# Kernel tuning notes

Measured on AMD Instinct MI355X. Metric: run time of the kernel, lower is better.

The kernel has to match this reference:

```python
import jax, jax.numpy as jnp
import numpy as np

N, E, G, S = 200000, 800000, 2048, 128
NUM_OPS, NUM_ETYPES, NUMERIC = 64, 4, 12
H, TEXT, VOCAB, OUT = 256, 64, 30000, 512
IN0 = 32 + NUMERIC  # 44


def _ln(h, eps=1e-5):
    # nn.LayerNorm with default (ones/zeros) affine, created fresh each forward
    m = h.mean(-1, keepdims=True)
    v = ((h - m) ** 2).mean(-1, keepdims=True)
    return (h - m) * jax.lax.rsqrt(v + eps)


def _leaky(v):
    return jnp.where(v > 0, v, 0.1 * v)  # LeakyReLU(0.1)


def setup_inputs() -> dict:
    key = jax.random.key(0)
    ks = jax.random.split(key, 40)
    x = jax.random.normal(ks[0], (N, 1 + NUMERIC), jnp.float32)
    x = x.at[:, 0].set(jax.random.randint(ks[1], (N,), 0, NUM_OPS).astype(jnp.float32))
    inp = {
        'x': x,
        'edge_index': jax.random.randint(ks[2], (2, E), 0, N),
        'edge_attr': jax.random.randint(ks[3], (E,), 0, NUM_ETYPES),
        'batch': jnp.sort(jax.random.randint(ks[4], (N,), 0, G)),
        'sql_ids': jax.random.randint(ks[5], (G, S), 0, VOCAB),
        'sql_mask': (jax.random.uniform(ks[6], (G, S)) > 0.3).astype(jnp.float32),
        'op_embed': jax.random.normal(ks[7], (NUM_OPS, 32), jnp.float32),
        'edge_embed': jax.random.normal(ks[8], (NUM_ETYPES, 16), jnp.float32),
        'token_embed': jax.random.normal(ks[9], (VOCAB, TEXT), jnp.float32).at[0].set(0.0),  # padding_idx=0
    }
    dims = [IN0, H, H]
    k = 10
    for i, d in enumerate(dims):
        inp[f'lin_w{i}'] = jax.random.normal(ks[k], (d, 16), jnp.float32) * 0.05; k += 1
        inp[f'lin_b{i}'] = jnp.zeros((d,), jnp.float32)
        inp[f'eps{i}'] = jnp.zeros((), jnp.float32)  # train_eps init 0
        inp[f'W1_{i}'] = jax.random.normal(ks[k], (H, d), jnp.float32) * 0.05; k += 1
        inp[f'b1_{i}'] = jnp.zeros((H,), jnp.float32)
        inp[f'W2_{i}'] = jax.random.normal(ks[k], (H, H), jnp.float32) * 0.05; k += 1
        inp[f'b2_{i}'] = jnp.zeros((H,), jnp.float32)
    inp['mW1'] = jax.random.normal(ks[k], (H, H + 3 + TEXT), jnp.float32) * 0.05; k += 1
    inp['mb1'] = jnp.zeros((H,), jnp.float32)
    inp['mW2'] = jax.random.normal(ks[k], (OUT, H), jnp.float32) * 0.05
    inp['mb2'] = jnp.zeros((OUT,), jnp.float32)
    return inp


def reference(x, edge_index, edge_attr, batch, sql_ids, sql_mask,
              op_embed, edge_embed, token_embed,
              lin_w0, lin_b0, eps0, W1_0, b1_0, W2_0, b2_0,
              lin_w1, lin_b1, eps1, W1_1, b1_1, W2_1, b2_1,
              lin_w2, lin_b2, eps2, W1_2, b1_2, W2_2, b2_2,
              mW1, mb1, mW2, mb2):
    op_ids = jnp.clip(x[:, 0].astype(jnp.int32), 0, NUM_OPS - 1)
    nums = x[:, 1:]
    e_idx = jnp.minimum(edge_attr, NUM_ETYPES - 1)  # clamp_max
    edge_emb = edge_embed[e_idx]                    # [E,16]
    h = jnp.concatenate([op_embed[op_ids], nums], 1)  # [N,44]
    src, dst = edge_index[0], edge_index[1]
    convs = [(lin_w0, lin_b0, eps0, W1_0, b1_0, W2_0, b2_0),
             (lin_w1, lin_b1, eps1, W1_1, b1_1, W2_1, b2_1),
             (lin_w2, lin_b2, eps2, W1_2, b1_2, W2_2, b2_2)]
    for (lw, lb, eps, W1, b1, W2, b2) in convs:
        h_in = h
        # GINEConv: msg = relu(x_j + Lin(edge_attr)); sum-aggregate at dst
        msg = jax.nn.relu(h[src] + edge_emb @ lw.T + lb)        # [E,d]
        aggr = jax.ops.segment_sum(msg, dst, num_segments=h.shape[0])
        z = (1.0 + eps) * h + aggr
        h = jax.nn.relu(z @ W1.T + b1) @ W2.T + b2              # conv MLP -> [N,H]
        h = _ln(h)
        h = _leaky(h + h_in) if h_in.shape[-1] == h.shape[-1] else _leaky(h)
    # graph pooling
    g = jax.ops.segment_sum(h, batch, num_segments=G)            # global_add_pool
    count = jax.ops.segment_sum(jnp.ones((h.shape[0],), h.dtype), batch, num_segments=G)
    denom = jnp.maximum(count, 1.0)                              # scatter_mean semantics
    fanout_mean = jax.ops.segment_sum(x[:, 5], batch, num_segments=G) / denom
    cost_mean = jax.ops.segment_sum(x[:, 4], batch, num_segments=G) / denom
    graph_sum = jnp.stack([count, fanout_mean, cost_mean], 1)    # [G,3]
    # text pooling (masked mean)
    emb = token_embed[sql_ids]                                   # [G,S,TEXT]
    summed = (emb * sql_mask[..., None]).sum(1)
    lengths = jnp.maximum(sql_mask.sum(1, keepdims=True), 1.0)
    text_feat = summed / lengths
    cat = jnp.concatenate([g, graph_sum, text_feat], 1)          # [G, H+3+TEXT]
    hid = _leaky(cat @ mW1.T + mb1)                              # Dropout(0.1) is identity in eval
    return hid @ mW2.T + mb2                                     # [G, OUT]
```

## Files before the change

kernel.cpp:

```cpp
#include <hip/hip_runtime.h>

#define NN 200000
#define EE 800000
#define GG 2048
#define NBLK ((NN + 255) / 256)

typedef __attribute__((ext_vector_type(8))) short short8;
typedef __attribute__((ext_vector_type(4))) float f32x4;

__device__ __forceinline__ float bf2f(ushort u){
  unsigned x = ((unsigned)u) << 16;
  return __uint_as_float(x);
}
__device__ __forceinline__ ushort f2bf(float f){
  unsigned x = __float_as_uint(f);
  x += 0x7fffu + ((x >> 16) & 1u);
  return (ushort)(x >> 16);
}

__device__ __forceinline__ void swz256(const float* __restrict__ W, ushort* __restrict__ o, int idx){
  int ks = idx >> 13, rem = idx & 8191;
  int j16 = rem >> 9, rem2 = rem & 511;
  int ln = rem2 >> 3, t = rem2 & 7;
  int row = j16*16 + (ln & 15);
  int k = ks*32 + (ln >> 4)*8 + t;
  o[idx] = f2bf(W[(size_t)row*256 + k]);
}

__global__ __launch_bounds__(256) void prep_k(
    const float* __restrict__ W10, const float* __restrict__ W20,
    const float* __restrict__ W11, const float* __restrict__ W21,
    const float* __restrict__ W12, const float* __restrict__ W22,
    const float* __restrict__ lw0, const float* __restrict__ lb0,
    const float* __restrict__ lw1, const float* __restrict__ lb1,
    const float* __restrict__ lw2, const float* __restrict__ lb2,
    const float* __restrict__ eE, const float* __restrict__ mW1,
    const float* __restrict__ mW2,
    ushort* __restrict__ wb10, ushort* __restrict__ wb20,
    ushort* __restrict__ wb11, ushort* __restrict__ wb21,
    ushort* __restrict__ wb12, ushort* __restrict__ wb22,
    ushort* __restrict__ mW1b, ushort* __restrict__ mW2b,
    float* __restrict__ eb)
{
  int b = blockIdx.x, tid = threadIdx.x;
  if (b < 64){
    int idx = b*256 + tid;
    int ks = idx >> 13, rem = idx & 8191;
    int j16 = rem >> 9, rem2 = rem & 511;
    int ln = rem2 >> 3, t = rem2 & 7;
    int row = j16*16 + (ln & 15);
    int k = ks*32 + (ln >> 4)*8 + t;
    wb10[idx] = (k < 44) ? f2bf(W10[row*44 + k]) : (ushort)0;
    return;
  }
  b -= 64;
  if (b < 256){ swz256(W20, wb20, b*256+tid); return; } b -= 256;
  if (b < 256){ swz256(W11, wb11, b*256+tid); return; } b -= 256;
  if (b < 256){ swz256(W21, wb21, b*256+tid); return; } b -= 256;
  if (b < 256){ swz256(W12, wb12, b*256+tid); return; } b -= 256;
  if (b < 256){ swz256(W22, wb22, b*256+tid); return; } b -= 256;
  if (b < 384){
    int idx = b*256 + tid; int o = idx / 384, k = idx - o*384;
    mW1b[idx] = (k < 323) ? f2bf(mW1[(size_t)o*323 + k]) : (ushort)0;
    return;
  }
  b -= 384;
  if (b < 512){ int idx = b*256+tid; mW2b[idx] = f2bf(mW2[idx]); return; } b -= 512;
  int li = b >> 2, t = b & 3;
  const float* lw = (li == 0) ? lw0 : ((li == 1) ? lw1 : lw2);
  const float* lb = (li == 0) ? lb0 : ((li == 1) ? lb1 : lb2);
  int d = (li == 0) ? 44 : 256;
  float v = 0.f;
  if (tid < d){
    float a = 0.f;
    #pragma unroll
    for (int j = 0; j < 16; j++) a += eE[t*16 + j] * lw[tid*16 + j];
    v = a + lb[tid];
  }
  eb[(li*4 + t)*256 + tid] = v;
}

__global__ __launch_bounds__(256) void build_h0_k(
    const float* __restrict__ x, const float* __restrict__ opE, ushort* __restrict__ h0)
{
  int idx = blockIdx.x*256 + threadIdx.x;
  int i = idx >> 6, c = idx & 63;
  float v = 0.f;
  if (c < 32){
    int op = (int)x[(size_t)i*13];
    op = op < 0 ? 0 : (op > 63 ? 63 : op);
    v = opE[op*32 + c];
  } else if (c < 44){
    v = x[(size_t)i*13 + (c - 31)];
  }
  h0[idx] = f2bf(v);
}

__global__ __launch_bounds__(256) void deg_k(const int* __restrict__ dst, int* __restrict__ D){
  int e = blockIdx.x*256 + threadIdx.x;
  atomicAdd(&D[dst[e]], 1);
}
__global__ __launch_bounds__(256) void scan1_k(int* __restrict__ D, int* __restrict__ bsum){
  __shared__ int s[256];
  int b = blockIdx.x, t = threadIdx.x, idx = b*256 + t;
  int v = (idx < NN) ? D[idx] : 0;
  s[t] = v; __syncthreads();
  for (int off = 1; off < 256; off <<= 1){
    int u = (t >= off) ? s[t-off] : 0;
    __syncthreads();
    s[t] += u;
    __syncthreads();
  }
  if (idx < NN) D[idx] = s[t] - v;
  if (t == 255) bsum[b] = s[255];
}
__global__ __launch_bounds__(256) void scan2_k(int* __restrict__ bsum){
  __shared__ int s[256];
  __shared__ int carry;
  int t = threadIdx.x;
  if (t == 0) carry = 0;
  __syncthreads();
  for (int c0 = 0; c0 < NBLK; c0 += 256){
    int idx = c0 + t;
    int v = (idx < NBLK) ? bsum[idx] : 0;
    s[t] = v; __syncthreads();
    for (int off = 1; off < 256; off <<= 1){
      int u = (t >= off) ? s[t-off] : 0;
      __syncthreads();
      s[t] += u;
      __syncthreads();
    }
    int ex = s[t] - v + carry;
    if (idx < NBLK) bsum[idx] = ex;
    int tot = s[255];
    __syncthreads();
    if (t == 0) carry += tot;
    __syncthreads();
  }
}
__global__ __launch_bounds__(256) void scan3_k(int* __restrict__ D, const int* __restrict__ bsum){
  int b = blockIdx.x, idx = b*256 + threadIdx.x;
  if (idx < NN) D[idx] += bsum[b];
}
__global__ __launch_bounds__(256) void fill_k(const int* __restrict__ src, const int* __restrict__ dst,
                                              const int* __restrict__ et, int* __restrict__ D,
                                              int* __restrict__ csr){
  int e = blockIdx.x*256 + threadIdx.x;
  int d = dst[e];
  int t = et[e]; t = t < 3 ? t : 3;
  int pos = atomicAdd(&D[d], 1);
  csr[pos] = src[e] | (t << 18);
}

template<int KD, int RESID>
__global__ __launch_bounds__(256) void layerf_k(
    const ushort* __restrict__ hsrc, const int* __restrict__ Dend, const int* __restrict__ csr,
    const float* __restrict__ ebL,
    const ushort* __restrict__ W1s, const float* __restrict__ b1,
    const ushort* __restrict__ W2s, const float* __restrict__ b2,
    const float* __restrict__ epsp, ushort* __restrict__ hout)
{
  __shared__ ushort ZT[32][264];
  __shared__ float ebs[1024];
  __shared__ float red1[32][4], red2[32][4], mnL[32], rsL[32];
  const int tid = threadIdx.x, lane = tid & 63, wv = tid >> 6;
  const int l15 = lane & 15, lq = lane >> 4;
  const int rowBase = blockIdx.x * 32;
  const float epv = 1.0f + epsp[0];

  for (int i = tid; i < 1024; i += 256) ebs[i] = ebL[i];
  __syncthreads();

  if (KD == 256){
    int c = lane * 4;
    #pragma unroll 1
    for (int it = 0; it < 8; it++){
      int rr = wv*8 + it;
      int r = rowBase + rr;
      const ushort4 hv = *(const ushort4*)(hsrc + (size_t)r*256 + c);
      float a0 = epv*bf2f(hv.x), a1 = epv*bf2f(hv.y), a2 = epv*bf2f(hv.z), a3 = epv*bf2f(hv.w);
      int st = (r == 0) ? 0 : Dend[r-1];
      int en = Dend[r];
      if (st < en){
        int p = csr[st];
        ushort4 sv = *(const ushort4*)(hsrc + (size_t)(p & 0x3FFFF)*256 + c);
        int tt = (p >> 18)*256;
        for (int e = st; e < en; e++){
          ushort4 cur = sv; int tc = tt;
          int e2 = (e+1 < en) ? e+1 : e;
          int p2 = csr[e2];
          sv = *(const ushort4*)(hsrc + (size_t)(p2 & 0x3FFFF)*256 + c);
          tt = (p2 >> 18)*256;
          float v;
          v = bf2f(cur.x) + ebs[tc + c];     a0 += v > 0.f ? v : 0.f;
          v = bf2f(cur.y) + ebs[tc + c + 1]; a1 += v > 0.f ? v : 0.f;
          v = bf2f(cur.z) + ebs[tc + c + 2]; a2 += v > 0.f ? v : 0.f;
          v = bf2f(cur.w) + ebs[tc + c + 3]; a3 += v > 0.f ? v : 0.f;
        }
      }
      ushort4 o; o.x=f2bf(a0); o.y=f2bf(a1); o.z=f2bf(a2); o.w=f2bf(a3);
      *(ushort4*)&ZT[rr][c] = o;
    }
  } else {
    int c = l15 * 4;
    #pragma unroll 1
    for (int it = 0; it < 2; it++){
      int rr = wv*8 + it*4 + lq;
      int r = rowBase + rr;
      const ushort4 hv = *(const ushort4*)(hsrc + (size_t)r*64 + c);
      float a0 = epv*bf2f(hv.x), a1 = epv*bf2f(hv.y), a2 = epv*bf2f(hv.z), a3 = epv*bf2f(hv.w);
      int st = (r == 0) ? 0 : Dend[r-1];
      int en = Dend[r];
      if (st < en){
        int p = csr[st];
        ushort4 sv = *(const ushort4*)(hsrc + (size_t)(p & 0x3FFFF)*64 + c);
        int tt = (p >> 18)*256;
        for (int e = st; e < en; e++){
          ushort4 cur = sv; int tc = tt;
          int e2 = (e+1 < en) ? e+1 : e;
          int p2 = csr[e2];
          sv = *(const ushort4*)(hsrc + (size_t)(p2 & 0x3FFFF)*64 + c);
          tt = (p2 >> 18)*256;
          float v;
          v = bf2f(cur.x) + ebs[tc + c];     a0 += v > 0.f ? v : 0.f;
          v = bf2f(cur.y) + ebs[tc + c + 1]; a1 += v > 0.f ? v : 0.f;
          v = bf2f(cur.z) + ebs[tc + c + 2]; a2 += v > 0.f ? v : 0.f;
          v = bf2f(cur.w) + ebs[tc + c + 3]; a3 += v > 0.f ? v : 0.f;
        }
      }
      ushort4 o; o.x=f2bf(a0); o.y=f2bf(a1); o.z=f2bf(a2); o.w=f2bf(a3);
      *(ushort4*)&ZT[rr][c] = o;
    }
  }
  __syncthreads();

  f32x4 acc[2][4];
  #pragma unroll
  for (int i = 0; i < 2; i++)
    #pragma unroll
    for (int j = 0; j < 4; j++){ f32x4 z = {0.f,0.f,0.f,0.f}; acc[i][j] = z; }

  #pragma unroll
  for (int s = 0; s < KD/32; s++){
    short8 af[2], bfv[4];
    #pragma unroll
    for (int j = 0; j < 4; j++)
      bfv[j] = *(const short8*)(W1s + ((size_t)(s*16 + wv*4 + j)*64 + lane)*8);
    #pragma unroll
    for (int i = 0; i < 2; i++)
      af[i] = *(const short8*)&ZT[i*16 + l15][s*32 + lq*8];
    #pragma unroll
    for (int i = 0; i < 2; i++)
      #pragma unroll
      for (int j = 0; j < 4; j++)
        acc[i][j] = __builtin_amdgcn_mfma_f32_16x16x32_bf16(af[i], bfv[j], acc[i][j], 0, 0, 0);
  }
  __syncthreads();

  {
    float b1c[4];
    #pragma unroll
    for (int j = 0; j < 4; j++) b1c[j] = b1[wv*64 + j*16 + l15];
    #pragma unroll
    for (int i = 0; i < 2; i++)
      #pragma unroll
      for (int j = 0; j < 4; j++){
        int cc = wv*64 + j*16 + l15;
        #pragma unroll
        for (int rg = 0; rg < 4; rg++){
          int r = i*16 + (lq << 2) + rg;
          float v = acc[i][j][rg] + b1c[j];
          v = v > 0.f ? v : 0.f;
          ZT[r][cc] = f2bf(v);
        }
      }
  }
  __syncthreads();

  #pragma unroll
  for (int i = 0; i < 2; i++)
    #pragma unroll
    for (int j = 0; j < 4; j++){ f32x4 z = {0.f,0.f,0.f,0.f}; acc[i][j] = z; }

  #pragma unroll
  for (int s = 0; s < 8; s++){
    short8 af[2], bfv[4];
    #pragma unroll
    for (int j = 0; j < 4; j++)
      bfv[j] = *(const short8*)(W2s + ((size_t)(s*16 + wv*4 + j)*64 + lane)*8);
    #pragma unroll
    for (int i = 0; i < 2; i++)
      af[i] = *(const short8*)&ZT[i*16 + l15][s*32 + lq*8];
    #pragma unroll
    for (int i = 0; i < 2; i++)
      #pragma unroll
      for (int j = 0; j < 4; j++)
        acc[i][j] = __builtin_amdgcn_mfma_f32_16x16x32_bf16(af[i], bfv[j], acc[i][j], 0, 0, 0);
  }

  float b2c[4];
  #pragma unroll
  for (int j = 0; j < 4; j++) b2c[j] = b2[wv*64 + j*16 + l15];
  #pragma unroll
  for (int i = 0; i < 2; i++){
    #pragma unroll
    for (int rg = 0; rg < 4; rg++){
      float s1 = 0.f, s2 = 0.f;
      #pragma unroll
      for (int j = 0; j < 4; j++){
        float y = acc[i][j][rg] + b2c[j];
        s1 += y; s2 += y*y;
      }
      #pragma unroll
      for (int m = 1; m < 16; m <<= 1){
        s1 += __shfl_xor(s1, m, 64);
        s2 += __shfl_xor(s2, m, 64);
      }
      if (l15 == 0){
        int r = i*16 + (lq << 2) + rg;
        red1[r][wv] = s1; red2[r][wv] = s2;
      }
    }
  }
  __syncthreads();
  if (tid < 32){
    float s1 = red1[tid][0] + red1[tid][1] + red1[tid][2] + red1[tid][3];
    float s2 = red2[tid][0] + red2[tid][1] + red2[tid][2] + red2[tid][3];
    float mn = s1 * (1.f/256.f);
    float vr = s2 * (1.f/256.f) - mn*mn;
    mnL[tid] = mn;
    rsL[tid] = rsqrtf(vr + 1e-5f);
  }
  __syncthreads();
  #pragma unroll
  for (int i = 0; i < 2; i++){
    #pragma unroll
    for (int rg = 0; rg < 4; rg++){
      int r = i*16 + (lq << 2) + rg;
      float mn = mnL[r], rs = rsL[r];
      #pragma unroll
      for (int j = 0; j < 4; j++){
        int cc = wv*64 + j*16 + l15;
        float y = acc[i][j][rg] + b2c[j];
        float v = (y - mn) * rs;
        if (RESID) v += bf2f(hsrc[(size_t)(rowBase + r)*256 + cc]);
        v = v > 0.f ? v : 0.1f*v;
        ZT[r][cc] = f2bf(v);
      }
    }
  }
  __syncthreads();
  #pragma unroll
  for (int p = 0; p < 8; p++){
    int r = p*4 + (tid >> 6);
    int c = (tid & 63) * 4;
    *(ushort4*)(hout + (size_t)(rowBase + r)*256 + c) = *(const ushort4*)&ZT[r][c];
  }
}

__global__ __launch_bounds__(256) void readout_k(
    const ushort* __restrict__ h, const int* __restrict__ batch, const float* __restrict__ x,
    const int* __restrict__ sqlIds, const float* __restrict__ sqlMask,
    const float* __restrict__ tok, ushort* __restrict__ catb)
{
  int g = blockIdx.x, tid = threadIdx.x;
  __shared__ int se[2];
  __shared__ float part[4][64];
  __shared__ float mpart[4];
  if (tid < 2){
    int target = g + tid;
    int lo = 0, hi = NN;
    while (lo < hi){ int mid = (lo + hi) >> 1; if (batch[mid] < target) lo = mid + 1; else hi = mid; }
    se[tid] = lo;
  }
  __syncthreads();
  int start = se[0], end = se[1];
  float a = 0.f;
  for (int i = start; i < end; i++) a += bf2f(h[(size_t)i*256 + tid]);
  catb[(size_t)g*384 + tid] = f2bf(a);
  if (tid < 2){
    int col = (tid == 0) ? 5 : 4;
    float s = 0.f;
    for (int i = start; i < end; i++) s += x[(size_t)i*13 + col];
    float cnt = (float)(end - start);
    float dn = cnt > 1.f ? cnt : 1.f;
    if (tid == 0){ catb[(size_t)g*384 + 256] = f2bf(cnt); catb[(size_t)g*384 + 257] = f2bf(s / dn); }
    else { catb[(size_t)g*384 + 258] = f2bf(s / dn); }
  }
  int grp = tid >> 6, c = tid & 63;
  float acc = 0.f, m = 0.f;
  for (int s = grp; s < 128; s += 4){
    int id = sqlIds[g*128 + s];
    float mk = sqlMask[g*128 + s];
    m += mk;
    acc += tok[(size_t)id*64 + c] * mk;
  }
  part[grp][c] = acc;
  if (c == 0) mpart[grp] = m;
  __syncthreads();
  if (tid < 64){
    float L = mpart[0] + mpart[1] + mpart[2] + mpart[3];
    L = L > 1.f ? L : 1.f;
    float tsum = part[0][tid] + part[1][tid] + part[2][tid] + part[3][tid];
    catb[(size_t)g*384 + 259 + tid] = f2bf(tsum / L);
  }
  if (tid >= 64 && tid < 125){
    catb[(size_t)g*384 + 259 + tid] = 0;
  }
}

__global__ __launch_bounds__(256) void head1_k(
    const ushort* __restrict__ catb, const ushort* __restrict__ W1b,
    const float* __restrict__ b1, ushort* __restrict__ hidb)
{
  __shared__ ushort smem[64*72 + 256*72];
  ushort (*As)[72] = (ushort(*)[72])smem;
  ushort (*Ws)[72] = (ushort(*)[72])(smem + 64*72);
  const int tid = threadIdx.x, lane = tid & 63, wv = tid >> 6;
  const int rowBase = blockIdx.x * 64;
  f32x4 acc[4][4];
  #pragma unroll
  for (int i = 0; i < 4; i++)
    #pragma unroll
    for (int j = 0; j < 4; j++){ f32x4 z = {0.f,0.f,0.f,0.f}; acc[i][j] = z; }

  for (int k0 = 0; k0 < 384; k0 += 64){
    __syncthreads();
    #pragma unroll
    for (int p = 0; p < 4; p++){
      int r = p*16 + (tid >> 4);
      int kk = (tid & 15) * 4;
      *(ushort4*)&As[r][kk] = *(const ushort4*)(catb + (size_t)(rowBase + r)*384 + k0 + kk);
    }
    #pragma unroll
    for (int p = 0; p < 16; p++){
      int oc = p*16 + (tid >> 4);
      int kk = (tid & 15) * 4;
      *(ushort4*)&Ws[oc][kk] = *(const ushort4*)(W1b + (size_t)oc*384 + k0 + kk);
    }
    __syncthreads();
    #pragma unroll
    for (int kc = 0; kc < 2; kc++){
      short8 af[4], bfv[4];
      #pragma unroll
      for (int i = 0; i < 4; i++)
        af[i] = *(const short8*)&As[i*16 + (lane & 15)][kc*32 + (lane >> 4)*8];
      #pragma unroll
      for (int j = 0; j < 4; j++)
        bfv[j] = *(const short8*)&Ws[wv*64 + j*16 + (lane & 15)][kc*32 + (lane >> 4)*8];
      #pragma unroll
      for (int i = 0; i < 4; i++)
        #pragma unroll
        for (int j = 0; j < 4; j++)
          acc[i][j] = __builtin_amdgcn_mfma_f32_16x16x32_bf16(af[i], bfv[j], acc[i][j], 0, 0, 0);
    }
  }
  __syncthreads();
  ushort (*Cs)[264] = (ushort(*)[264])smem;
  #pragma unroll
  for (int j = 0; j < 4; j++){
    int cc = wv*64 + j*16 + (lane & 15);
    float bb = b1[cc];
    #pragma unroll
    for (int i = 0; i < 4; i++){
      #pragma unroll
      for (int rg = 0; rg < 4; rg++){
        int r = i*16 + ((lane >> 4) << 2) + rg;
        float v = acc[i][j][rg] + bb;
        v = v > 0.f ? v : 0.1f*v;
        Cs[r][cc] = f2bf(v);
      }
    }
  }
  __syncthreads();
  #pragma unroll
  for (int p = 0; p < 16; p++){
    int r = p*4 + (tid >> 6);
    int c = (tid & 63) * 4;
    *(ushort4*)(hidb + (size_t)(rowBase + r)*256 + c) = *(const ushort4*)&Cs[r][c];
  }
}

__global__ __launch_bounds__(256) void head2_k(
    const ushort* __restrict__ hidb, const ushort* __restrict__ W2b,
    const float* __restrict__ b2, float* __restrict__ out)
{
  __shared__ float smemf[128*132];
  ushort (*As)[72] = (ushort(*)[72])smemf;
  ushort (*Bs)[72] = (ushort(*)[72])((ushort*)smemf + 128*72);
  const int tid = threadIdx.x, lane = tid & 63, wv = tid >> 6;
  const int wr = (wv >> 1) * 64;
  const int wc = (wv & 1) * 64;
  const int rowBase = blockIdx.x * 128;
  const int colBase = blockIdx.y * 128;
  const int lr = tid >> 4, lk = (tid & 15) * 4;

  f32x4 acc[4][4];
  #pragma unroll
  for (int i = 0; i < 4; i++)
    #pragma unroll
    for (int j = 0; j < 4; j++){ f32x4 z = {0.f,0.f,0.f,0.f}; acc[i][j] = z; }

  for (int k0 = 0; k0 < 256; k0 += 64){
    __syncthreads();
    #pragma unroll
    for (int p = 0; p < 8; p++){
      int r = lr + p*16;
      *(ushort4*)&As[r][lk] = *(const ushort4*)(hidb + (size_t)(rowBase + r)*256 + k0 + lk);
      *(ushort4*)&Bs[r][lk] = *(const ushort4*)(W2b + (size_t)(colBase + r)*256 + k0 + lk);
    }
    __syncthreads();
    #pragma unroll
    for (int kc = 0; kc < 2; kc++){
      short8 af[4], bfv[4];
      #pragma unroll
      for (int i = 0; i < 4; i++)
        af[i] = *(const short8*)&As[wr + i*16 + (lane & 15)][kc*32 + (lane >> 4)*8];
      #pragma unroll
      for (int j = 0; j < 4; j++)
        bfv[j] = *(const short8*)&Bs[wc + j*16 + (lane & 15)][kc*32 + (lane >> 4)*8];
      #pragma unroll
      for (int i = 0; i < 4; i++)
        #pragma unroll
        for (int j = 0; j < 4; j++)
          acc[i][j] = __builtin_amdgcn_mfma_f32_16x16x32_bf16(af[i], bfv[j], acc[i][j], 0, 0, 0);
    }
  }
  __syncthreads();
  float (*Cs)[132] = (float(*)[132])smemf;
  #pragma unroll
  for (int j = 0; j < 4; j++){
    int cl = wc + j*16 + (lane & 15);
    float bb = b2[colBase + cl];
    #pragma unroll
    for (int i = 0; i < 4; i++){
      int r0 = wr + i*16 + ((lane >> 4) << 2);
      #pragma unroll
      for (int rg = 0; rg < 4; rg++)
        Cs[r0 + rg][cl] = acc[i][j][rg] + bb;
    }
  }
  __syncthreads();
  #pragma unroll
  for (int p = 0; p < 16; p++){
    int r = (tid >> 5) + p*8;
    int c4 = (tid & 31) * 4;
    *(float4*)(out + (size_t)(rowBase + r)*512 + colBase + c4) = *(const float4*)&Cs[r][c4];
  }
}

extern "C" void kernel_launch(void* const* d_in, const int* in_sizes, int n_in,
                              void* d_out, int out_size, void* d_ws, size_t ws_size,
                              hipStream_t stream)
{
  const float* x       = (const float*)d_in[0];
  const int*   ei      = (const int*)d_in[1];
  const int*   src     = ei;
  const int*   dst     = ei + EE;
  const int*   eattr   = (const int*)d_in[2];
  const int*   batch   = (const int*)d_in[3];
  const int*   sqlIds  = (const int*)d_in[4];
  const float* sqlMask = (const float*)d_in[5];
  const float* opE     = (const float*)d_in[6];
  const float* eE      = (const float*)d_in[7];
  const float* tok     = (const float*)d_in[8];
  const float* lw0 = (const float*)d_in[9],  *lb0 = (const float*)d_in[10], *eps0 = (const float*)d_in[11];
  const float* W10 = (const float*)d_in[12], *b10 = (const float*)d_in[13];
  const float* W20 = (const float*)d_in[14], *b20 = (const float*)d_in[15];
  const float* lw1 = (const float*)d_in[16], *lb1 = (const float*)d_in[17], *eps1 = (const float*)d_in[18];
  const float* W11 = (const float*)d_in[19], *b11 = (const float*)d_in[20];
  const float* W21 = (const float*)d_in[21], *b21 = (const float*)d_in[22];
  const float* lw2 = (const float*)d_in[23], *lb2 = (const float*)d_in[24], *eps2 = (const float*)d_in[25];
  const float* W12 = (const float*)d_in[26], *b12 = (const float*)d_in[27];
  const float* W22 = (const float*)d_in[28], *b22 = (const float*)d_in[29];
  const float* mW1 = (const float*)d_in[30], *mb1 = (const float*)d_in[31];
  const float* mW2 = (const float*)d_in[32], *mb2 = (const float*)d_in[33];
  float* out = (float*)d_out;

  char* ws = (char*)d_ws;
  size_t off = 0;
  const size_t NB256 = (size_t)NN*256*2;
  ushort* bufH    = (ushort*)(ws + off); off += NB256;
  char*   region  = ws + off;            off += NB256;
  ushort* h0      = (ushort*)region;
  ushort* hPong   = (ushort*)region;
  ushort* catb    = (ushort*)region;
  ushort* hidb    = (ushort*)(region + (size_t)GG*384*2);
  ushort* wb10 = (ushort*)(ws + off); off += (size_t)256*64*2;
  ushort* wb20 = (ushort*)(ws + off); off += (size_t)65536*2;
  ushort* wb11 = (ushort*)(ws + off); off += (size_t)65536*2;
  ushort* wb21 = (ushort*)(ws + off); off += (size_t)65536*2;
  ushort* wb12 = (ushort*)(ws + off); off += (size_t)65536*2;
  ushort* wb22 = (ushort*)(ws + off); off += (size_t)65536*2;
  ushort* mW1b = (ushort*)(ws + off); off += (size_t)256*384*2;
  ushort* mW2b = (ushort*)(ws + off); off += (size_t)512*256*2;
  float*  eb   = (float*)(ws + off);  off += (size_t)3*4*256*4;
  int* D    = (int*)(ws + off); off += (size_t)NN*4;
  int* bsum = (int*)(ws + off); off += (size_t)NBLK*4;
  int* csr  = (int*)(ws + off); off += (size_t)EE*4;
  size_t needFast = off;

  if (ws_size < needFast) return;

  prep_k<<<2252, 256, 0, stream>>>(W10, W20, W11, W21, W12, W22,
                                   lw0, lb0, lw1, lb1, lw2, lb2, eE, mW1, mW2,
                                   wb10, wb20, wb11, wb21, wb12, wb22, mW1b, mW2b, eb);
  build_h0_k<<<50000, 256, 0, stream>>>(x, opE, h0);

  hipMemsetAsync(D, 0, (size_t)NN*4, stream);
  deg_k<<<3125, 256, 0, stream>>>(dst, D);
  scan1_k<<<NBLK, 256, 0, stream>>>(D, bsum);
  scan2_k<<<1, 256, 0, stream>>>(bsum);
  scan3_k<<<NBLK, 256, 0, stream>>>(D, bsum);
  fill_k<<<3125, 256, 0, stream>>>(src, dst, eattr, D, csr);

  layerf_k<64,0><<<6250, 256, 0, stream>>>(h0,    D, csr, eb,        wb10, b10, wb20, b20, eps0, bufH);
  layerf_k<256,1><<<6250, 256, 0, stream>>>(bufH, D, csr, eb + 1024, wb11, b11, wb21, b21, eps1, hPong);
  layerf_k<256,1><<<6250, 256, 0, stream>>>(hPong,D, csr, eb + 2048, wb12, b12, wb22, b22, eps2, bufH);

  readout_k<<<GG, 256, 0, stream>>>(bufH, batch, x, sqlIds, sqlMask, tok, catb);
  head1_k<<<32, 256, 0, stream>>>(catb, mW1b, mb1, hidb);
  head2_k<<<dim3(16, 4), 256, 0, stream>>>(hidb, mW2b, mb2, out);
}
```

Baseline: 960.7 us.

## Aggregate neighbors edge-parallel per block with LDS float atomics

Neighbor aggregation no longer walks each row's CSR range in its own loop. Each block now takes the contiguous edge range of its 32 rows and spreads those edges across its 4 waves. The local destination row is packed into spare csr bits, and messages are accumulated with float atomicAdd into an fp32 LDS tile. Edge embeddings are held in registers instead of an LDS table, and the tile is converted to bf16 when the first GEMM's A fragments are loaded. This aims to balance uneven per-row degrees across waves, at the cost of LDS atomics and narrower 2-byte per-lane gathers instead of 8-byte vector loads.

```diff
diff --git a/kernel.cpp b/kernel.cpp
--- a/kernel.cpp
+++ b/kernel.cpp
@@ -16,6 +16,12 @@
   unsigned x = __float_as_uint(f);
   x += 0x7fffu + ((x >> 16) & 1u);
   return (ushort)(x >> 16);
+}
+__device__ __forceinline__ short8 pack8(float4 a, float4 b){
+  short8 r;
+  r[0]=(short)f2bf(a.x); r[1]=(short)f2bf(a.y); r[2]=(short)f2bf(a.z); r[3]=(short)f2bf(a.w);
+  r[4]=(short)f2bf(b.x); r[5]=(short)f2bf(b.y); r[6]=(short)f2bf(b.z); r[7]=(short)f2bf(b.w);
+  return r;
 }
 
 __device__ __forceinline__ void swz256(const float* __restrict__ W, ushort* __restrict__ o, int idx){
@@ -149,7 +155,7 @@
   int d = dst[e];
   int t = et[e]; t = t < 3 ? t : 3;
   int pos = atomicAdd(&D[d], 1);
-  csr[pos] = src[e] | (t << 18);
+  csr[pos] = src[e] | (t << 18) | ((d & 31) << 20);
 }
 
 template<int KD, int RESID>
@@ -160,76 +166,56 @@
     const ushort* __restrict__ W2s, const float* __restrict__ b2,
     const float* __restrict__ epsp, ushort* __restrict__ hout)
 {
-  __shared__ ushort ZT[32][264];
-  __shared__ float ebs[1024];
+  __shared__ float AZ[32][264];
   __shared__ float red1[32][4], red2[32][4], mnL[32], rsL[32];
+  ushort* ZT = (ushort*)&AZ[0][0];
   const int tid = threadIdx.x, lane = tid & 63, wv = tid >> 6;
   const int l15 = lane & 15, lq = lane >> 4;
   const int rowBase = blockIdx.x * 32;
   const float epv = 1.0f + epsp[0];
-
-  for (int i = tid; i < 1024; i += 256) ebs[i] = ebL[i];
-  __syncthreads();
-
-  if (KD == 256){
-    int c = lane * 4;
-    #pragma unroll 1
-    for (int it = 0; it < 8; it++){
-      int rr = wv*8 + it;
-      int r = rowBase + rr;
-      const ushort4 hv = *(const ushort4*)(hsrc + (size_t)r*256 + c);
-      float a0 = epv*bf2f(hv.x), a1 = epv*bf2f(hv.y), a2 = epv*bf2f(hv.z), a3 = epv*bf2f(hv.w);
-      int st = (r == 0) ? 0 : Dend[r-1];
-      int en = Dend[r];
-      if (st < en){
-        int p = csr[st];
-        ushort4 sv = *(const ushort4*)(hsrc + (size_t)(p & 0x3FFFF)*256 + c);
-        int tt = (p >> 18)*256;
-        for (int e = st; e < en; e++){
-          ushort4 cur = sv; int tc = tt;
-          int e2 = (e+1 < en) ? e+1 : e;
-          int p2 = csr[e2];
-          sv = *(const ushort4*)(hsrc + (size_t)(p2 & 0x3FFFF)*256 + c);
-          tt = (p2 >> 18)*256;
-          float v;
-          v = bf2f(cur.x) + ebs[tc + c];     a0 += v > 0.f ? v : 0.f;
-          v = bf2f(cur.y) + ebs[tc + c + 1]; a1 += v > 0.f ? v : 0.f;
-          v = bf2f(cur.z) + ebs[tc + c + 2]; a2 += v > 0.f ? v : 0.f;
-          v = bf2f(cur.w) + ebs[tc + c + 3]; a3 += v > 0.f ? v : 0.f;
-        }
+  const int KV = (KD == 256) ? 4 : 1;
+
+  float ebv0[4], ebv1[4], ebv2[4], ebv3[4];
+  #pragma unroll
+  for (int k = 0; k < 4; k++){
+    if (k < KV){
+      ebv0[k] = ebL[0*256 + lane + 64*k];
+      ebv1[k] = ebL[1*256 + lane + 64*k];
+      ebv2[k] = ebL[2*256 + lane + 64*k];
+      ebv3[k] = ebL[3*256 + lane + 64*k];
+    } else { ebv0[k]=ebv1[k]=ebv2[k]=ebv3[k]=0.f; }
+  }
+
+  #pragma unroll
+  for (int it = 0; it < 8; it++){
+    int rr = it*4 + wv;
+    if (KD == 256){
+      #pragma unroll
+      for (int k = 0; k < 4; k++)
+        AZ[rr][lane + 64*k] = epv * bf2f(hsrc[(size_t)(rowBase + rr)*256 + lane + 64*k]);
+    } else {
+      AZ[rr][lane] = epv * bf2f(hsrc[(size_t)(rowBase + rr)*64 + lane]);
+    }
+  }
+  __syncthreads();
+
+  {
+    int e0 = (rowBase == 0) ? 0 : Dend[rowBase - 1];
+    int e1 = Dend[rowBase + 31];
+    #pragma unroll 2
+    for (int e = e0 + wv; e < e1; e += 4){
+      int p = csr[e];
+      int s = p & 0x3FFFF;
+      int tt = (p >> 18) & 3;
+      int lr = p >> 20;
+      #pragma unroll
+      for (int k = 0; k < KV; k++){
+        float ee = (tt == 0) ? ebv0[k] : (tt == 1) ? ebv1[k] : (tt == 2) ? ebv2[k] : ebv3[k];
+        float hv = bf2f(hsrc[(size_t)s*((KD==256)?256:64) + lane + 64*k]);
+        float v = hv + ee;
+        v = v > 0.f ? v : 0.f;
+        atomicAdd(&AZ[lr][lane + 64*k], v);
       }
-      ushort4 o; o.x=f2bf(a0); o.y=f2bf(a1); o.z=f2bf(a2); o.w=f2bf(a3);
-      *(ushort4*)&ZT[rr][c] = o;
-    }
-  } else {
-    int c = l15 * 4;
-    #pragma unroll 1
-    for (int it = 0; it < 2; it++){
-      int rr = wv*8 + it*4 + lq;
-      int r = rowBase + rr;
-      const ushort4 hv = *(const ushort4*)(hsrc + (size_t)r*64 + c);
-      float a0 = epv*bf2f(hv.x), a1 = epv*bf2f(hv.y), a2 = epv*bf2f(hv.z), a3 = epv*bf2f(hv.w);
-      int st = (r == 0) ? 0 : Dend[r-1];
-      int en = Dend[r];
-      if (st < en){
-        int p = csr[st];
-        ushort4 sv = *(const ushort4*)(hsrc + (size_t)(p & 0x3FFFF)*64 + c);
-        int tt = (p >> 18)*256;
-        for (int e = st; e < en; e++){
-          ushort4 cur = sv; int tc = tt;
-          int e2 = (e+1 < en) ? e+1 : e;
-          int p2 = csr[e2];
-          sv = *(const ushort4*)(hsrc + (size_t)(p2 & 0x3FFFF)*64 + c);
-          tt = (p2 >> 18)*256;
-          float v;
-          v = bf2f(cur.x) + ebs[tc + c];     a0 += v > 0.f ? v : 0.f;
-          v = bf2f(cur.y) + ebs[tc + c + 1]; a1 += v > 0.f ? v : 0.f;
-          v = bf2f(cur.z) + ebs[tc + c + 2]; a2 += v > 0.f ? v : 0.f;
-          v = bf2f(cur.w) + ebs[tc + c + 3]; a3 += v > 0.f ? v : 0.f;
-        }
-      }
-      ushort4 o; o.x=f2bf(a0); o.y=f2bf(a1); o.z=f2bf(a2); o.w=f2bf(a3);
-      *(ushort4*)&ZT[rr][c] = o;
     }
   }
   __syncthreads();
@@ -247,8 +233,11 @@
     for (int j = 0; j < 4; j++)
       bfv[j] = *(const short8*)(W1s + ((size_t)(s*16 + wv*4 + j)*64 + lane)*8);
     #pragma unroll
-    for (int i = 0; i < 2; i++)
-      af[i] = *(const short8*)&ZT[i*16 + l15][s*32 + lq*8];
+    for (int i = 0; i < 2; i++){
+      const float4 f0 = *(const float4*)&AZ[i*16 + l15][s*32 + lq*8];
+      const float4 f1 = *(const float4*)&AZ[i*16 + l15][s*32 + lq*8 + 4];
+      af[i] = pack8(f0, f1);
+    }
     #pragma unroll
     for (int i = 0; i < 2; i++)
       #pragma unroll
@@ -271,7 +260,7 @@
           int r = i*16 + (lq << 2) + rg;
           float v = acc[i][j][rg] + b1c[j];
           v = v > 0.f ? v : 0.f;
-          ZT[r][cc] = f2bf(v);
+          ZT[r*264 + cc] = f2bf(v);
         }
       }
   }
@@ -290,7 +279,7 @@
       bfv[j] = *(const short8*)(W2s + ((size_t)(s*16 + wv*4 + j)*64 + lane)*8);
     #pragma unroll
     for (int i = 0; i < 2; i++)
-      af[i] = *(const short8*)&ZT[i*16 + l15][s*32 + lq*8];
+      af[i] = *(const short8*)&ZT[(i*16 + l15)*264 + s*32 + lq*8];
     #pragma unroll
     for (int i = 0; i < 2; i++)
       #pragma unroll
@@ -345,7 +334,7 @@
         float v = (y - mn) * rs;
         if (RESID) v += bf2f(hsrc[(size_t)(rowBase + r)*256 + cc]);
         v = v > 0.f ? v : 0.1f*v;
-        ZT[r][cc] = f2bf(v);
+        ZT[r*264 + cc] = f2bf(v);
       }
     }
   }
@@ -354,7 +343,7 @@
   for (int p = 0; p < 8; p++){
     int r = p*4 + (tid >> 6);
     int c = (tid & 63) * 4;
-    *(ushort4*)(hout + (size_t)(rowBase + r)*256 + c) = *(const ushort4*)&ZT[r][c];
+    *(ushort4*)(hout + (size_t)(rowBase + r)*256 + c) = *(const ushort4*)&ZT[r*264 + c];
   }
 }
 
```

After: 2.932 ms. 205% more time.

## Interleave neighbor gathers across four rows and cache residual rows in LDS

Applied to the files above, without the earlier changes.

The 256-wide aggregation loop now handles four destination rows together. Each of the four rows keeps its own prefetched neighbor load, so more independent global gathers are in flight per wave. The residual input rows are staged in shared memory during that first load, which removes a second global read in the epilogue. Edge-embedding reads are vectorized as float4, and the 64-wide path uses a compact edge-embedding table. The cost is extra LDS and register pressure, which may lower occupancy, plus branch divergence when the four rows have different degrees.

```diff
diff --git a/kernel.cpp b/kernel.cpp
--- a/kernel.cpp
+++ b/kernel.cpp
@@ -161,6 +161,7 @@
     const float* __restrict__ epsp, ushort* __restrict__ hout)
 {
   __shared__ ushort ZT[32][264];
+  __shared__ ushort HT[RESID ? 32 : 1][RESID ? 264 : 8];
   __shared__ float ebs[1024];
   __shared__ float red1[32][4], red2[32][4], mnL[32], rsL[32];
   const int tid = threadIdx.x, lane = tid & 63, wv = tid >> 6;
@@ -168,38 +169,99 @@
   const int rowBase = blockIdx.x * 32;
   const float epv = 1.0f + epsp[0];
 
-  for (int i = tid; i < 1024; i += 256) ebs[i] = ebL[i];
+  if (KD == 256){
+    for (int i = tid; i < 1024; i += 256) ebs[i] = ebL[i];
+  } else {
+    if (tid < 256) ebs[tid] = ebL[(tid >> 6)*256 + (tid & 63)];
+  }
   __syncthreads();
 
   if (KD == 256){
     int c = lane * 4;
     #pragma unroll 1
-    for (int it = 0; it < 8; it++){
-      int rr = wv*8 + it;
-      int r = rowBase + rr;
-      const ushort4 hv = *(const ushort4*)(hsrc + (size_t)r*256 + c);
-      float a0 = epv*bf2f(hv.x), a1 = epv*bf2f(hv.y), a2 = epv*bf2f(hv.z), a3 = epv*bf2f(hv.w);
-      int st = (r == 0) ? 0 : Dend[r-1];
-      int en = Dend[r];
-      if (st < en){
-        int p = csr[st];
-        ushort4 sv = *(const ushort4*)(hsrc + (size_t)(p & 0x3FFFF)*256 + c);
-        int tt = (p >> 18)*256;
-        for (int e = st; e < en; e++){
-          ushort4 cur = sv; int tc = tt;
-          int e2 = (e+1 < en) ? e+1 : e;
-          int p2 = csr[e2];
-          sv = *(const ushort4*)(hsrc + (size_t)(p2 & 0x3FFFF)*256 + c);
-          tt = (p2 >> 18)*256;
+    for (int it = 0; it < 2; it++){
+      int rr0 = wv*8 + it*4;
+      int r0 = rowBase + rr0;
+      float4 A0, A1, A2, A3;
+      {
+        ushort4 q0 = *(const ushort4*)(hsrc + (size_t)(r0+0)*256 + c);
+        ushort4 q1 = *(const ushort4*)(hsrc + (size_t)(r0+1)*256 + c);
+        ushort4 q2 = *(const ushort4*)(hsrc + (size_t)(r0+2)*256 + c);
+        ushort4 q3 = *(const ushort4*)(hsrc + (size_t)(r0+3)*256 + c);
+        if (RESID){
+          *(ushort4*)&HT[rr0+0][c] = q0;
+          *(ushort4*)&HT[rr0+1][c] = q1;
+          *(ushort4*)&HT[rr0+2][c] = q2;
+          *(ushort4*)&HT[rr0+3][c] = q3;
+        }
+        A0 = make_float4(epv*bf2f(q0.x), epv*bf2f(q0.y), epv*bf2f(q0.z), epv*bf2f(q0.w));
+        A1 = make_float4(epv*bf2f(q1.x), epv*bf2f(q1.y), epv*bf2f(q1.z), epv*bf2f(q1.w));
+        A2 = make_float4(epv*bf2f(q2.x), epv*bf2f(q2.y), epv*bf2f(q2.z), epv*bf2f(q2.w));
+        A3 = make_float4(epv*bf2f(q3.x), epv*bf2f(q3.y), epv*bf2f(q3.z), epv*bf2f(q3.w));
+      }
+      int bm1 = (r0 == 0) ? 0 : Dend[r0-1];
+      int e0 = Dend[r0], e1 = Dend[r0+1], e2 = Dend[r0+2], e3 = Dend[r0+3];
+      int st0 = bm1, st1 = e0, st2 = e1, st3 = e2;
+      int n0 = e0 - st0, n1 = e1 - st1, n2 = e2 - st2, n3 = e3 - st3;
+      int nmax = n0 > n1 ? n0 : n1;
+      nmax = nmax > n2 ? nmax : n2;
+      nmax = nmax > n3 ? nmax : n3;
+      ushort4 z4; z4.x = z4.y = z4.z = z4.w = 0;
+      ushort4 sv0 = z4, sv1 = z4, sv2 = z4, sv3 = z4;
+      int t0 = 0, t1 = 0, t2 = 0, t3 = 0;
+      if (n0 > 0){ int p = csr[st0]; sv0 = *(const ushort4*)(hsrc + (size_t)(p & 0x3FFFF)*256 + c); t0 = ((p >> 18) & 3)*256; }
+      if (n1 > 0){ int p = csr[st1]; sv1 = *(const ushort4*)(hsrc + (size_t)(p & 0x3FFFF)*256 + c); t1 = ((p >> 18) & 3)*256; }
+      if (n2 > 0){ int p = csr[st2]; sv2 = *(const ushort4*)(hsrc + (size_t)(p & 0x3FFFF)*256 + c); t2 = ((p >> 18) & 3)*256; }
+      if (n3 > 0){ int p = csr[st3]; sv3 = *(const ushort4*)(hsrc + (size_t)(p & 0x3FFFF)*256 + c); t3 = ((p >> 18) & 3)*256; }
+      for (int k = 0; k < nmax; k++){
+        ushort4 c0 = sv0, c1 = sv1, c2 = sv2, c3 = sv3;
+        int u0 = t0, u1 = t1, u2 = t2, u3 = t3;
+        if (k+1 < n0){ int p = csr[st0+k+1]; sv0 = *(const ushort4*)(hsrc + (size_t)(p & 0x3FFFF)*256 + c); t0 = ((p >> 18) & 3)*256; }
+        if (k+1 < n1){ int p = csr[st1+k+1]; sv1 = *(const ushort4*)(hsrc + (size_t)(p & 0x3FFFF)*256 + c); t1 = ((p >> 18) & 3)*256; }
+        if (k+1 < n2){ int p = csr[st2+k+1]; sv2 = *(const ushort4*)(hsrc + (size_t)(p & 0x3FFFF)*256 + c); t2 = ((p >> 18) & 3)*256; }
+        if (k+1 < n3){ int p = csr[st3+k+1]; sv3 = *(const ushort4*)(hsrc + (size_t)(p & 0x3FFFF)*256 + c); t3 = ((p >> 18) & 3)*256; }
+        if (k < n0){
+          const float4 ev = *(const float4*)&ebs[u0 + c];
           float v;
-          v = bf2f(cur.x) + ebs[tc + c];     a0 += v > 0.f ? v : 0.f;
-          v = bf2f(cur.y) + ebs[tc + c + 1]; a1 += v > 0.f ? v : 0.f;
-          v = bf2f(cur.z) + ebs[tc + c + 2]; a2 += v > 0.f ? v : 0.f;
-          v = bf2f(cur.w) + ebs[tc + c + 3]; a3 += v > 0.f ? v : 0.f;
+          v = bf2f(c0.x) + ev.x; A0.x += v > 0.f ? v : 0.f;
+          v = bf2f(c0.y) + ev.y; A0.y += v > 0.f ? v : 0.f;
+          v = bf2f(c0.z) + ev.z; A0.z += v > 0.f ? v : 0.f;
+          v = bf2f(c0.w) + ev.w; A0.w += v > 0.f ? v : 0.f;
         }
-      }
-      ushort4 o; o.x=f2bf(a0); o.y=f2bf(a1); o.z=f2bf(a2); o.w=f2bf(a3);
-      *(ushort4*)&ZT[rr][c] = o;
+        if (k < n1){
+          const float4 ev = *(const float4*)&ebs[u1 + c];
+          float v;
+          v = bf2f(c1.x) + ev.x; A1.x += v > 0.f ? v : 0.f;
+          v = bf2f(c1.y) + ev.y; A1.y += v > 0.f ? v : 0.f;
+          v = bf2f(c1.z) + ev.z; A1.z += v > 0.f ? v : 0.f;
+          v = bf2f(c1.w) + ev.w; A1.w += v > 0.f ? v : 0.f;
+        }
+        if (k < n2){
+          const float4 ev = *(const float4*)&ebs[u2 + c];
+          float v;
+          v = bf2f(c2.x) + ev.x; A2.x += v > 0.f ? v : 0.f;
+          v = bf2f(c2.y) + ev.y; A2.y += v > 0.f ? v : 0.f;
+          v = bf2f(c2.z) + ev.z; A2.z += v > 0.f ? v : 0.f;
+          v = bf2f(c2.w) + ev.w; A2.w += v > 0.f ? v : 0.f;
+        }
+        if (k < n3){
+          const float4 ev = *(const float4*)&ebs[u3 + c];
+          float v;
+          v = bf2f(c3.x) + ev.x; A3.x += v > 0.f ? v : 0.f;
+          v = bf2f(c3.y) + ev.y; A3.y += v > 0.f ? v : 0.f;
+          v = bf2f(c3.z) + ev.z; A3.z += v > 0.f ? v : 0.f;
+          v = bf2f(c3.w) + ev.w; A3.w += v > 0.f ? v : 0.f;
+        }
+      }
+      ushort4 o;
+      o.x = f2bf(A0.x); o.y = f2bf(A0.y); o.z = f2bf(A0.z); o.w = f2bf(A0.w);
+      *(ushort4*)&ZT[rr0+0][c] = o;
+      o.x = f2bf(A1.x); o.y = f2bf(A1.y); o.z = f2bf(A1.z); o.w = f2bf(A1.w);
+      *(ushort4*)&ZT[rr0+1][c] = o;
+      o.x = f2bf(A2.x); o.y = f2bf(A2.y); o.z = f2bf(A2.z); o.w = f2bf(A2.w);
+      *(ushort4*)&ZT[rr0+2][c] = o;
+      o.x = f2bf(A3.x); o.y = f2bf(A3.y); o.z = f2bf(A3.z); o.w = f2bf(A3.w);
+      *(ushort4*)&ZT[rr0+3][c] = o;
     }
   } else {
     int c = l15 * 4;
@@ -214,18 +276,19 @@
       if (st < en){
         int p = csr[st];
         ushort4 sv = *(const ushort4*)(hsrc + (size_t)(p & 0x3FFFF)*64 + c);
-        int tt = (p >> 18)*256;
+        int tt = ((p >> 18) & 3)*64;
         for (int e = st; e < en; e++){
           ushort4 cur = sv; int tc = tt;
           int e2 = (e+1 < en) ? e+1 : e;
           int p2 = csr[e2];
           sv = *(const ushort4*)(hsrc + (size_t)(p2 & 0x3FFFF)*64 + c);
-          tt = (p2 >> 18)*256;
+          tt = ((p2 >> 18) & 3)*64;
+          const float4 ev = *(const float4*)&ebs[tc + c];
           float v;
-          v = bf2f(cur.x) + ebs[tc + c];     a0 += v > 0.f ? v : 0.f;
-          v = bf2f(cur.y) + ebs[tc + c + 1]; a1 += v > 0.f ? v : 0.f;
-          v = bf2f(cur.z) + ebs[tc + c + 2]; a2 += v > 0.f ? v : 0.f;
-          v = bf2f(cur.w) + ebs[tc + c + 3]; a3 += v > 0.f ? v : 0.f;
+          v = bf2f(cur.x) + ev.x; a0 += v > 0.f ? v : 0.f;
+          v = bf2f(cur.y) + ev.y; a1 += v > 0.f ? v : 0.f;
+          v = bf2f(cur.z) + ev.z; a2 += v > 0.f ? v : 0.f;
+          v = bf2f(cur.w) + ev.w; a3 += v > 0.f ? v : 0.f;
         }
       }
       ushort4 o; o.x=f2bf(a0); o.y=f2bf(a1); o.z=f2bf(a2); o.w=f2bf(a3);
@@ -343,7 +406,7 @@
         int cc = wv*64 + j*16 + l15;
         float y = acc[i][j][rg] + b2c[j];
         float v = (y - mn) * rs;
-        if (RESID) v += bf2f(hsrc[(size_t)(rowBase + r)*256 + cc]);
+        if (RESID) v += bf2f(HT[r][cc]);
         v = v > 0.f ? v : 0.1f*v;
         ZT[r][cc] = f2bf(v);
       }
```

Result: faster. 884.1 us (-8.0%).
